# Kernel tuning notes

Measured on AMD Instinct MI355X. Metric: run time of the kernel, lower is better.

## Reference

```python
import jax, jax.numpy as jnp
import numpy as np
from jax import lax

# dims from init_kwargs: in_features=1920, out_features=1920, window_size=12
B = 1024
IN_F = 1920
OUT_F = 1920
WS = 12              # window_size (GRU input & hidden size)
K = IN_F // WS
OUT_WS = OUT_F // K  # per-block decoder output = 12
D_HID = 1024         # decoder hidden width


def sinusoidal_pe(L, d):
    # standard sinusoidal positional encoding, shape (L, d)
    pos = jnp.arange(L, dtype=jnp.float32)[:, None]
    div = jnp.exp(jnp.arange(0, d, 2, dtype=jnp.float32) * (-np.log(10000.0) / d))
    ang = pos * div  # (L, d//2)
    pe = jnp.zeros((L, d), jnp.float32)
    pe = pe.at[:, 0::2].set(jnp.sin(ang))
    pe = pe.at[:, 1::2].set(jnp.cos(ang))
    return pe


def gru(x, h0, Wih, Whh, bih, bhh):
    # x: (B, T, I) batch_first; PyTorch GRU gate order: r, z, n
    def step(h, xt):
        gi = xt @ Wih.T + bih          # (B, 3H)
        gh = h @ Whh.T + bhh           # (B, 3H)
        ir, iz, inn = jnp.split(gi, 3, axis=-1)
        hr, hz, hn = jnp.split(gh, 3, axis=-1)
        r = jax.nn.sigmoid(ir + hr)
        z = jax.nn.sigmoid(iz + hz)
        n = jnp.tanh(inn + r * hn)
        h_new = (1.0 - z) * n + z * h
        return h_new, h_new
    hT, ys = lax.scan(step, h0, jnp.swapaxes(x, 0, 1))
    return jnp.swapaxes(ys, 0, 1), hT


def setup_inputs() -> dict:
    key = jax.random.key(0)
    ks = jax.random.split(key, 11)
    s = lambda k, shape: jax.random.normal(k, shape, jnp.float32) * 0.05
    return {
        "x": jax.random.normal(ks[0], (B, IN_F), jnp.float32),
        # per-block segment encoders: Linear(WS, WS) x K
        "enc_W": s(ks[1], (K, WS, WS)),
        "enc_b": s(ks[2], (K, WS)),
        # shared GRU (input=hidden=WS)
        "Wih": s(ks[3], (3 * WS, WS)),
        "Whh": s(ks[4], (3 * WS, WS)),
        "bih": s(ks[5], (3 * WS,)),
        "bhh": s(ks[6], (3 * WS,)),
        # per-block decoders: Linear(WS,1024) -> Linear(1024,OUT_WS)
        "dec_W1": s(ks[7], (K, WS, D_HID)),
        "dec_b1": s(ks[8], (K, D_HID)),
        "dec_W2": s(ks[9], (K, D_HID, OUT_WS)),
        "dec_b2": s(ks[10], (K, OUT_WS)),
    }


def reference(x, enc_W, enc_b, Wih, Whh, bih, bhh, dec_W1, dec_b1, dec_W2, dec_b2):
    # SegmentationBlock: split (B, IN_F) -> (B, K, WS), per-block Linear+ReLU
    xb = x.reshape(B, K, WS)
    xs = jax.nn.relu(jnp.einsum('bki,kio->bko', xb, enc_W) + enc_b[None])

    # first GRU pass: only final hidden state h (B, WS)
    h0 = jnp.zeros((B, WS), x.dtype)
    _, h = gru(xs, h0, Wih, Whh, bih, bhh)

    # positional encodings (value-independent sinusoidal, broadcast over batch)
    pos_enc = sinusoidal_pe(K, WS)          # (K, WS)
    ch_pe = sinusoidal_pe(K, K)             # (K, K)
    # channel_enc[:, :, j] = channel_encs[:, :, j // K]  (fused gather)
    channel_enc = ch_pe[:, jnp.arange(WS) // K]  # (K, WS)

    x_enc = xs + pos_enc[None] + channel_enc[None]

    # second GRU pass initialized with h
    out, _ = gru(x_enc, h, Wih, Whh, bih, bhh)  # (B, K, WS)

    # per-block decoder MLPs (dropout is identity in eval)
    hid = jnp.einsum('bkd,kdh->bkh', out, dec_W1) + dec_b1[None]      # (B, K, 1024)
    res = jnp.einsum('bkh,kho->bko', hid, dec_W2) + dec_b2[None]      # (B, K, OUT_WS)
    return res.reshape(B, K * OUT_WS)[:, :OUT_F]
```

## Files before the change

### kernel.cpp

```cpp
#include <hip/hip_runtime.h>
#include <hip/hip_bf16.h>

using bf16 = __hip_bfloat16;

#define C1 1.44269504f
#define C2 2.88539008f

__device__ __forceinline__ float fexp2(float x) { return __builtin_amdgcn_exp2f(x); }
__device__ __forceinline__ float frcp(float x)  { return __builtin_amdgcn_rcpf(x); }

__device__ __forceinline__ unsigned int f2bfbits(float f) {
    union { float f; unsigned int u; } c; c.f = f;
    return (c.u + 0x7fffu + ((c.u >> 16) & 1u)) >> 16;
}

#define KSTR 12288
#define OFF_PEGI 15728640
#define OFF_WC   15759360

__global__ __launch_bounds__(256) void k_encode(
    const float* __restrict__ x, const float* __restrict__ encW, const float* __restrict__ encb,
    const float* __restrict__ Wih, const float* __restrict__ bih, const float* __restrict__ bhh,
    uint2* __restrict__ gi, float4* __restrict__ pegi)
{
    const int k = blockIdx.y, t = threadIdx.x;
    const int b = blockIdx.x * 256 + t;

    __shared__ float sW[144], sbm[12], sWih[432], sbih[36], spet[12];
    __shared__ uint2 st[256 * 13];
    if (t < 144) sW[t]  = encW[k * 144 + t];
    if (t < 12)  sbm[t] = encb[k * 12 + t];
    for (int i = t; i < 432; i += 256) sWih[i] = Wih[i];
    if (t < 36)  sbih[t] = bih[t] + (t < 24 ? bhh[t] : 0.f);
    if (t < 12) {
        int m = t >> 1;
        float div = __expf((float)(2 * m) * (-0.7675283643313489f));
        float ang = (float)k * div;
        spet[t] = ((t & 1) ? cosf(ang) : sinf(ang)) + sinf((float)k);
    }
    __syncthreads();
    if (t < 12 && blockIdx.x == 0) {
        float sr = 0.f, sz = 0.f, sn = 0.f;
        #pragma unroll
        for (int o = 0; o < 12; o++) {
            sr = fmaf(spet[o], sWih[t * 12 + o], sr);
            sz = fmaf(spet[o], sWih[(12 + t) * 12 + o], sz);
            sn = fmaf(spet[o], sWih[(24 + t) * 12 + o], sn);
        }
        pegi[k * 12 + t] = make_float4(C1 * sr, C1 * sz, C2 * sn, 0.f);
    }

    const float4* xp = reinterpret_cast<const float4*>(x + (size_t)b * 1920 + k * 12);
    float4 a0 = xp[0], a1 = xp[1], a2 = xp[2];
    float xv[12] = {a0.x,a0.y,a0.z,a0.w, a1.x,a1.y,a1.z,a1.w, a2.x,a2.y,a2.z,a2.w};

    float xs[12];
    #pragma unroll
    for (int o = 0; o < 12; o++) {
        float s = sbm[o];
        #pragma unroll
        for (int i = 0; i < 12; i++) s = fmaf(xv[i], sW[i * 12 + o], s);
        xs[o] = fmaxf(s, 0.f);
    }

    #pragma unroll
    for (int j = 0; j < 12; j++) {
        float sr = sbih[j], sz = sbih[12 + j], sn = sbih[24 + j];
        #pragma unroll
        for (int o = 0; o < 12; o++) {
            sr = fmaf(xs[o], sWih[j * 12 + o], sr);
            sz = fmaf(xs[o], sWih[(12 + j) * 12 + o], sz);
            sn = fmaf(xs[o], sWih[(24 + j) * 12 + o], sn);
        }
        st[t * 13 + j] = make_uint2(f2bfbits(C1 * sr) | (f2bfbits(C1 * sz) << 16),
                                    f2bfbits(C2 * sn));
    }
    __syncthreads();
    uint2* gbase = gi + (size_t)k * KSTR + (size_t)blockIdx.x * 3072;
    for (int i = t; i < 3072; i += 256) {
        int bl = i / 12;
        gbase[i] = st[bl * 13 + (i - bl * 12)];
    }
}

__global__ __launch_bounds__(64) void k_recur(
    const float* __restrict__ Whh, const float* __restrict__ bhh,
    const uint2* __restrict__ gi, const float4* __restrict__ pegi,
    float* __restrict__ hout)
{
    const int lane = threadIdx.x;
    const int ju = (lane < 12) ? lane : 11;
    const int b = blockIdx.x;

    float wr[12], wz[12], wn[12];
    #pragma unroll
    for (int d = 0; d < 12; d++) {
        wr[d] = C1 * Whh[ju * 12 + d];
        wz[d] = C1 * Whh[(12 + ju) * 12 + d];
        wn[d] = C2 * Whh[(24 + ju) * 12 + d];
    }
    const float bn = C2 * bhh[24 + ju];

    const uint2* gp = gi + (size_t)b * 12 + ju;

    float hs[12];
    #pragma unroll
    for (int d = 0; d < 12; d++) hs[d] = 0.f;
    float hself = 0.f, p = 1.f;

    uint2 buf[8];
    #pragma unroll
    for (int i = 0; i < 8; i++) buf[i] = gp[(size_t)i * KSTR];

    for (int ko = 0; ko < 160; ko += 8) {
        #pragma unroll
        for (int i = 0; i < 8; i++) {
            const int k = ko + i;
            const int kp = (k + 8 > 159) ? 159 : k + 8;
            float hr = __int_as_float((int)(buf[i].x << 16));
            float hz = __int_as_float((int)(buf[i].x & 0xffff0000u));
            float gn = __int_as_float((int)(buf[i].y << 16));
            buf[i] = gp[(size_t)kp * KSTR];
            float hn = bn;
            #pragma unroll
            for (int d = 0; d < 12; d++) {
                hr = fmaf(wr[d], hs[d], hr);
                hz = fmaf(wz[d], hs[d], hz);
                hn = fmaf(wn[d], hs[d], hn);
            }
            float w = frcp(1.f + fexp2(hz));
            float r = frcp(1.f + fexp2(-hr));
            float t = fmaf(r, hn, gn);
            float e = frcp(1.f + fexp2(t));
            float hj = fmaf(w, fmaf(-2.f, e, p), hself);
            hself = hj; p = 1.f - hj;
            int hv = __float_as_int(hj);
            #pragma unroll
            for (int d = 0; d < 12; d++)
                hs[d] = __int_as_float(__builtin_amdgcn_readlane(hv, d));
        }
    }

    const float4* pp = pegi + ju;
    float4 pb[8];
    #pragma unroll
    for (int i = 0; i < 8; i++) {
        buf[i] = gp[(size_t)i * KSTR];
        pb[i]  = pp[i * 12];
    }
    float* ho = hout + (size_t)b * 1920;
    for (int ko = 0; ko < 160; ko += 8) {
        #pragma unroll
        for (int i = 0; i < 8; i++) {
            const int k = ko + i;
            const int kp = (k + 8 > 159) ? 159 : k + 8;
            float hr = __int_as_float((int)(buf[i].x << 16))         + pb[i].x;
            float hz = __int_as_float((int)(buf[i].x & 0xffff0000u)) + pb[i].y;
            float gn = __int_as_float((int)(buf[i].y << 16))         + pb[i].z;
            buf[i] = gp[(size_t)kp * KSTR];
            pb[i]  = pp[kp * 12];
            float hn = bn;
            #pragma unroll
            for (int d = 0; d < 12; d++) {
                hr = fmaf(wr[d], hs[d], hr);
                hz = fmaf(wz[d], hs[d], hz);
                hn = fmaf(wn[d], hs[d], hn);
            }
            float w = frcp(1.f + fexp2(hz));
            float r = frcp(1.f + fexp2(-hr));
            float t = fmaf(r, hn, gn);
            float e = frcp(1.f + fexp2(t));
            float hj = fmaf(w, fmaf(-2.f, e, p), hself);
            hself = hj; p = 1.f - hj;
            if (lane < 12) ho[k * 12 + lane] = hj;
            int hv = __float_as_int(hj);
            #pragma unroll
            for (int d = 0; d < 12; d++)
                hs[d] = __int_as_float(__builtin_amdgcn_readlane(hv, d));
        }
    }
}

__global__ __launch_bounds__(256) void k_fold(
    const float* __restrict__ W1, const float* __restrict__ b1,
    const float* __restrict__ W2, const float* __restrict__ b2,
    float* __restrict__ Wcg)
{
    const int k = blockIdx.x, t = threadIdx.x;
    __shared__ float sB[12288];
    __shared__ float sb1[1024];
    {
        const float4* w2p = reinterpret_cast<const float4*>(W2 + (size_t)k * 12288);
        float4* sB4 = reinterpret_cast<float4*>(sB);
        for (int i = t; i < 3072; i += 256) sB4[i] = w2p[i];
        const float4* b1p = reinterpret_cast<const float4*>(b1 + (size_t)k * 1024);
        float4* sb14 = reinterpret_cast<float4*>(sb1);
        if (t < 256) sb14[t] = b1p[t];
    }
    __syncthreads();
    if (t >= 156) return;
    const int o = (t < 144) ? (t % 12) : (t - 144);
    float s0 = 0.f, s1 = 0.f, s2 = 0.f, s3 = 0.f;
    if (t < 144) {
        const float4* va4 = reinterpret_cast<const float4*>(W1 + (size_t)k * 12288 + (size_t)(t / 12) * 1024);
        #pragma unroll 4
        for (int q = 0; q < 256; q++) {
            float4 a = va4[q];
            const float* bq = sB + q * 48 + o;
            s0 = fmaf(a.x, bq[0],  s0);
            s1 = fmaf(a.y, bq[12], s1);
            s2 = fmaf(a.z, bq[24], s2);
            s3 = fmaf(a.w, bq[36], s3);
        }
    } else {
        #pragma unroll 4
        for (int hh = 0; hh < 1024; hh += 4) {
            const float* bq = sB + hh * 12 + o;
            s0 = fmaf(sb1[hh],     bq[0],  s0);
            s1 = fmaf(sb1[hh + 1], bq[12], s1);
            s2 = fmaf(sb1[hh + 2], bq[24], s2);
            s3 = fmaf(sb1[hh + 3], bq[36], s3);
        }
    }
    float s = (s0 + s1) + (s2 + s3);
    if (t >= 144) s += b2[k * 12 + o];
    Wcg[k * 156 + t] = s;
}

__global__ __launch_bounds__(256) void k_apply(
    const float* __restrict__ Wcg, float* __restrict__ out)
{
    const int k = blockIdx.x, t = threadIdx.x;
    __shared__ float sw[156];
    if (t < 156) sw[t] = Wcg[k * 156 + t];
    __syncthreads();

    for (int bb = t; bb < 1024; bb += 256) {
        float* hp = out + (size_t)bb * 1920 + k * 12;
        float4* h4 = reinterpret_cast<float4*>(hp);
        float4 a0 = h4[0], a1 = h4[1], a2 = h4[2];
        float hv[12] = {a0.x,a0.y,a0.z,a0.w, a1.x,a1.y,a1.z,a1.w, a2.x,a2.y,a2.z,a2.w};
        float ov[12];
        #pragma unroll
        for (int o = 0; o < 12; o++) {
            float s = sw[144 + o];
            #pragma unroll
            for (int d = 0; d < 12; d++) s = fmaf(hv[d], sw[d * 12 + o], s);
            ov[o] = s;
        }
        h4[0] = make_float4(ov[0], ov[1], ov[2],  ov[3]);
        h4[1] = make_float4(ov[4], ov[5], ov[6],  ov[7]);
        h4[2] = make_float4(ov[8], ov[9], ov[10], ov[11]);
    }
}

extern "C" void kernel_launch(void* const* d_in, const int* in_sizes, int n_in,
                              void* d_out, int out_size, void* d_ws, size_t ws_size,
                              hipStream_t stream)
{
    const float* x    = (const float*)d_in[0];
    const float* encW = (const float*)d_in[1];
    const float* encb = (const float*)d_in[2];
    const float* Wih  = (const float*)d_in[3];
    const float* Whh  = (const float*)d_in[4];
    const float* bih  = (const float*)d_in[5];
    const float* bhh  = (const float*)d_in[6];
    const float* W1   = (const float*)d_in[7];
    const float* b1   = (const float*)d_in[8];
    const float* W2   = (const float*)d_in[9];
    const float* b2   = (const float*)d_in[10];
    float* out = (float*)d_out;

    char* ws = (char*)d_ws;
    uint2*  gi   = (uint2*)(ws);
    float4* pegi = (float4*)(ws + OFF_PEGI);
    float*  Wcg  = (float*)(ws + OFF_WC);

    k_encode<<<dim3(4, 160), 256, 0, stream>>>(x, encW, encb, Wih, bih, bhh, gi, pegi);
    k_fold  <<<dim3(160),    256, 0, stream>>>(W1, b1, W2, b2, Wcg);
    k_recur <<<dim3(1024),   64,  0, stream>>>(Whh, bhh, gi, pegi, out);
    k_apply <<<dim3(160),    256, 0, stream>>>(Wcg, out);
}
```

Baseline: 202.7 us.

## Vectorize GRU recurrence with packed float2 FMAs and fuse fold into apply

The GRU hidden-state matvec in the recurrent kernel now uses 2-wide float vectors so the compiler can emit packed FMA instructions, halving the FMA count on the serial critical path. Separately, the decoder weight-folding kernel is merged with the apply kernel: the folded 12x12 weights and bias go to shared memory instead of a global workspace, which removes one launch and one round trip. The trade-off is that the fold now runs after the recurrence instead of overlapping or preceding it, and the split accumulators add a final horizontal add per gate.

```diff
diff --git a/kernel.cpp b/kernel.cpp
--- a/kernel.cpp
+++ b/kernel.cpp
@@ -2,6 +2,7 @@
 #include <hip/hip_bf16.h>
 
 using bf16 = __hip_bfloat16;
+typedef float v2f __attribute__((ext_vector_type(2)));
 
 #define C1 1.44269504f
 #define C2 2.88539008f
@@ -16,7 +17,6 @@
 
 #define KSTR 12288
 #define OFF_PEGI 15728640
-#define OFF_WC   15759360
 
 __global__ __launch_bounds__(256) void k_encode(
     const float* __restrict__ x, const float* __restrict__ encW, const float* __restrict__ encb,
@@ -92,20 +92,20 @@
     const int ju = (lane < 12) ? lane : 11;
     const int b = blockIdx.x;
 
-    float wr[12], wz[12], wn[12];
-    #pragma unroll
-    for (int d = 0; d < 12; d++) {
-        wr[d] = C1 * Whh[ju * 12 + d];
-        wz[d] = C1 * Whh[(12 + ju) * 12 + d];
-        wn[d] = C2 * Whh[(24 + ju) * 12 + d];
+    v2f wr2[6], wz2[6], wn2[6];
+    #pragma unroll
+    for (int i = 0; i < 6; i++) {
+        wr2[i] = (v2f){C1 * Whh[ju * 12 + 2*i],        C1 * Whh[ju * 12 + 2*i + 1]};
+        wz2[i] = (v2f){C1 * Whh[(12 + ju) * 12 + 2*i], C1 * Whh[(12 + ju) * 12 + 2*i + 1]};
+        wn2[i] = (v2f){C2 * Whh[(24 + ju) * 12 + 2*i], C2 * Whh[(24 + ju) * 12 + 2*i + 1]};
     }
     const float bn = C2 * bhh[24 + ju];
 
     const uint2* gp = gi + (size_t)b * 12 + ju;
 
-    float hs[12];
-    #pragma unroll
-    for (int d = 0; d < 12; d++) hs[d] = 0.f;
+    v2f hs2[6];
+    #pragma unroll
+    for (int i = 0; i < 6; i++) hs2[i] = (v2f){0.f, 0.f};
     float hself = 0.f, p = 1.f;
 
     uint2 buf[8];
@@ -117,27 +117,31 @@
         for (int i = 0; i < 8; i++) {
             const int k = ko + i;
             const int kp = (k + 8 > 159) ? 159 : k + 8;
-            float hr = __int_as_float((int)(buf[i].x << 16));
-            float hz = __int_as_float((int)(buf[i].x & 0xffff0000u));
+            float gr = __int_as_float((int)(buf[i].x << 16));
+            float gz = __int_as_float((int)(buf[i].x & 0xffff0000u));
             float gn = __int_as_float((int)(buf[i].y << 16));
             buf[i] = gp[(size_t)kp * KSTR];
-            float hn = bn;
-            #pragma unroll
-            for (int d = 0; d < 12; d++) {
-                hr = fmaf(wr[d], hs[d], hr);
-                hz = fmaf(wz[d], hs[d], hz);
-                hn = fmaf(wn[d], hs[d], hn);
-            }
+            v2f an = (v2f){bn, 0.f};
+            v2f ar = (v2f){gr, 0.f};
+            v2f az = (v2f){gz, 0.f};
+            #pragma unroll
+            for (int d = 0; d < 6; d++) an += wn2[d] * hs2[d];
+            #pragma unroll
+            for (int d = 0; d < 6; d++) { ar += wr2[d] * hs2[d]; az += wz2[d] * hs2[d]; }
+            float hr = ar.x + ar.y;
+            float hz = az.x + az.y;
+            float hn = an.x + an.y;
+            float r = frcp(1.f + fexp2(-hr));
             float w = frcp(1.f + fexp2(hz));
-            float r = frcp(1.f + fexp2(-hr));
             float t = fmaf(r, hn, gn);
             float e = frcp(1.f + fexp2(t));
             float hj = fmaf(w, fmaf(-2.f, e, p), hself);
             hself = hj; p = 1.f - hj;
             int hv = __float_as_int(hj);
             #pragma unroll
-            for (int d = 0; d < 12; d++)
-                hs[d] = __int_as_float(__builtin_amdgcn_readlane(hv, d));
+            for (int d = 0; d < 6; d++)
+                hs2[d] = (v2f){__int_as_float(__builtin_amdgcn_readlane(hv, 2*d)),
+                               __int_as_float(__builtin_amdgcn_readlane(hv, 2*d + 1))};
         }
     }
 
@@ -154,20 +158,23 @@
         for (int i = 0; i < 8; i++) {
             const int k = ko + i;
             const int kp = (k + 8 > 159) ? 159 : k + 8;
-            float hr = __int_as_float((int)(buf[i].x << 16))         + pb[i].x;
-            float hz = __int_as_float((int)(buf[i].x & 0xffff0000u)) + pb[i].y;
+            float gr = __int_as_float((int)(buf[i].x << 16))         + pb[i].x;
+            float gz = __int_as_float((int)(buf[i].x & 0xffff0000u)) + pb[i].y;
             float gn = __int_as_float((int)(buf[i].y << 16))         + pb[i].z;
             buf[i] = gp[(size_t)kp * KSTR];
             pb[i]  = pp[kp * 12];
-            float hn = bn;
-            #pragma unroll
-            for (int d = 0; d < 12; d++) {
-                hr = fmaf(wr[d], hs[d], hr);
-                hz = fmaf(wz[d], hs[d], hz);
-                hn = fmaf(wn[d], hs[d], hn);
-            }
+            v2f an = (v2f){bn, 0.f};
+            v2f ar = (v2f){gr, 0.f};
+            v2f az = (v2f){gz, 0.f};
+            #pragma unroll
+            for (int d = 0; d < 6; d++) an += wn2[d] * hs2[d];
+            #pragma unroll
+            for (int d = 0; d < 6; d++) { ar += wr2[d] * hs2[d]; az += wz2[d] * hs2[d]; }
+            float hr = ar.x + ar.y;
+            float hz = az.x + az.y;
+            float hn = an.x + an.y;
+            float r = frcp(1.f + fexp2(-hr));
             float w = frcp(1.f + fexp2(hz));
-            float r = frcp(1.f + fexp2(-hr));
             float t = fmaf(r, hn, gn);
             float e = frcp(1.f + fexp2(t));
             float hj = fmaf(w, fmaf(-2.f, e, p), hself);
@@ -175,64 +182,59 @@
             if (lane < 12) ho[k * 12 + lane] = hj;
             int hv = __float_as_int(hj);
             #pragma unroll
-            for (int d = 0; d < 12; d++)
-                hs[d] = __int_as_float(__builtin_amdgcn_readlane(hv, d));
-        }
-    }
-}
-
-__global__ __launch_bounds__(256) void k_fold(
+            for (int d = 0; d < 6; d++)
+                hs2[d] = (v2f){__int_as_float(__builtin_amdgcn_readlane(hv, 2*d)),
+                               __int_as_float(__builtin_amdgcn_readlane(hv, 2*d + 1))};
+        }
+    }
+}
+
+__global__ __launch_bounds__(256) void k_foldapply(
     const float* __restrict__ W1, const float* __restrict__ b1,
     const float* __restrict__ W2, const float* __restrict__ b2,
-    float* __restrict__ Wcg)
+    float* __restrict__ out)
 {
     const int k = blockIdx.x, t = threadIdx.x;
     __shared__ float sB[12288];
     __shared__ float sb1[1024];
+    __shared__ float sWc[144], sbc[12];
     {
         const float4* w2p = reinterpret_cast<const float4*>(W2 + (size_t)k * 12288);
         float4* sB4 = reinterpret_cast<float4*>(sB);
         for (int i = t; i < 3072; i += 256) sB4[i] = w2p[i];
         const float4* b1p = reinterpret_cast<const float4*>(b1 + (size_t)k * 1024);
         float4* sb14 = reinterpret_cast<float4*>(sb1);
-        if (t < 256) sb14[t] = b1p[t];
-    }
-    __syncthreads();
-    if (t >= 156) return;
-    const int o = (t < 144) ? (t % 12) : (t - 144);
-    float s0 = 0.f, s1 = 0.f, s2 = 0.f, s3 = 0.f;
-    if (t < 144) {
-        const float4* va4 = reinterpret_cast<const float4*>(W1 + (size_t)k * 12288 + (size_t)(t / 12) * 1024);
-        #pragma unroll 4
-        for (int q = 0; q < 256; q++) {
-            float4 a = va4[q];
-            const float* bq = sB + q * 48 + o;
-            s0 = fmaf(a.x, bq[0],  s0);
-            s1 = fmaf(a.y, bq[12], s1);
-            s2 = fmaf(a.z, bq[24], s2);
-            s3 = fmaf(a.w, bq[36], s3);
-        }
-    } else {
-        #pragma unroll 4
-        for (int hh = 0; hh < 1024; hh += 4) {
-            const float* bq = sB + hh * 12 + o;
-            s0 = fmaf(sb1[hh],     bq[0],  s0);
-            s1 = fmaf(sb1[hh + 1], bq[12], s1);
-            s2 = fmaf(sb1[hh + 2], bq[24], s2);
-            s3 = fmaf(sb1[hh + 3], bq[36], s3);
-        }
-    }
-    float s = (s0 + s1) + (s2 + s3);
-    if (t >= 144) s += b2[k * 12 + o];
-    Wcg[k * 156 + t] = s;
-}
-
-__global__ __launch_bounds__(256) void k_apply(
-    const float* __restrict__ Wcg, float* __restrict__ out)
-{
-    const int k = blockIdx.x, t = threadIdx.x;
-    __shared__ float sw[156];
-    if (t < 156) sw[t] = Wcg[k * 156 + t];
+        sb14[t] = b1p[t];
+    }
+    __syncthreads();
+    if (t < 156) {
+        const int o = (t < 144) ? (t % 12) : (t - 144);
+        float s0 = 0.f, s1 = 0.f, s2 = 0.f, s3 = 0.f;
+        if (t < 144) {
+            const float4* va4 = reinterpret_cast<const float4*>(W1 + (size_t)k * 12288 + (size_t)(t / 12) * 1024);
+            #pragma unroll 4
+            for (int q = 0; q < 256; q++) {
+                float4 a = va4[q];
+                const float* bq = sB + q * 48 + o;
+                s0 = fmaf(a.x, bq[0],  s0);
+                s1 = fmaf(a.y, bq[12], s1);
+                s2 = fmaf(a.z, bq[24], s2);
+                s3 = fmaf(a.w, bq[36], s3);
+            }
+        } else {
+            #pragma unroll 4
+            for (int hh = 0; hh < 1024; hh += 4) {
+                const float* bq = sB + hh * 12 + o;
+                s0 = fmaf(sb1[hh],     bq[0],  s0);
+                s1 = fmaf(sb1[hh + 1], bq[12], s1);
+                s2 = fmaf(sb1[hh + 2], bq[24], s2);
+                s3 = fmaf(sb1[hh + 3], bq[36], s3);
+            }
+        }
+        float s = (s0 + s1) + (s2 + s3);
+        if (t < 144) sWc[t] = s;
+        else         sbc[t - 144] = s + b2[k * 12 + o];
+    }
     __syncthreads();
 
     for (int bb = t; bb < 1024; bb += 256) {
@@ -243,9 +245,9 @@
         float ov[12];
         #pragma unroll
         for (int o = 0; o < 12; o++) {
-            float s = sw[144 + o];
-            #pragma unroll
-            for (int d = 0; d < 12; d++) s = fmaf(hv[d], sw[d * 12 + o], s);
+            float s = sbc[o];
+            #pragma unroll
+            for (int d = 0; d < 12; d++) s = fmaf(hv[d], sWc[d * 12 + o], s);
             ov[o] = s;
         }
         h4[0] = make_float4(ov[0], ov[1], ov[2],  ov[3]);
@@ -274,10 +276,8 @@
     char* ws = (char*)d_ws;
     uint2*  gi   = (uint2*)(ws);
     float4* pegi = (float4*)(ws + OFF_PEGI);
-    float*  Wcg  = (float*)(ws + OFF_WC);
-
-    k_encode<<<dim3(4, 160), 256, 0, stream>>>(x, encW, encb, Wih, bih, bhh, gi, pegi);
-    k_fold  <<<dim3(160),    256, 0, stream>>>(W1, b1, W2, b2, Wcg);
-    k_recur <<<dim3(1024),   64,  0, stream>>>(Whh, bhh, gi, pegi, out);
-    k_apply <<<dim3(160),    256, 0, stream>>>(Wcg, out);
-}
+
+    k_encode   <<<dim3(4, 160), 256, 0, stream>>>(x, encW, encb, Wih, bih, bhh, gi, pegi);
+    k_recur    <<<dim3(1024),   64,  0, stream>>>(Whh, bhh, gi, pegi, out);
+    k_foldapply<<<dim3(160),    256, 0, stream>>>(W1, b1, W2, b2, out);
+}
```

After: 188.3 us. -7.1%, faster.
